# Kernel optimization log

Hardware: AMD Instinct MI355X
Metric: run time of the kernel (lower is better)

The kernel has to match this reference:

```python
import jax, jax.numpy as jnp
import numpy as np
import math

B_CH = 128   # bottleneck channels (conv1x1 in)
N_CH = 256   # encoder filters (conv1x1 out / linear in)
L = 16       # filter length (linear out); hop = L//2
BATCH = 8
K = 32000    # number of frames
T_ORIGIN = (L // 2) * (K - 1) + L  # 256008


def setup_inputs() -> dict:
    key = jax.random.key(0)
    k1, k2, k3, k4 = jax.random.split(key, 4)
    return {
        "mixture_w": jax.random.normal(k1, (BATCH, N_CH, K), jnp.float32),
        "est_mask": jax.random.normal(k2, (BATCH, B_CH, K), jnp.float32),
        "W_mask": jax.random.normal(k3, (N_CH, B_CH), jnp.float32) * (1.0 / np.sqrt(B_CH)),
        "W_basis": jax.random.normal(k4, (L, N_CH), jnp.float32) * (1.0 / np.sqrt(N_CH)),
        "T_origin": T_ORIGIN,
    }


def overlap_and_add(signal, frame_step):
    # signal: [..., frames, frame_length]
    frames, frame_length = signal.shape[-2], signal.shape[-1]
    sub_len = math.gcd(frame_length, frame_step)
    sub_step = frame_step // sub_len
    spf = frame_length // sub_len  # subframes per frame
    out_size = frame_step * (frames - 1) + frame_length
    out_sub = out_size // sub_len
    sub_sig = signal.reshape(signal.shape[:-2] + (frames * spf, sub_len))
    # scatter index for each subframe (same as torch unfold + index_add_)
    idx = (jnp.arange(frames)[:, None] * sub_step + jnp.arange(spf)[None, :]).reshape(-1)
    res = jnp.zeros(signal.shape[:-2] + (out_sub, sub_len), signal.dtype)
    res = res.at[..., idx, :].add(sub_sig)
    return res.reshape(signal.shape[:-2] + (out_size,))


def reference(mixture_w, est_mask, W_mask, W_basis, T_origin):
    # conv1x1 (bias-free) == channel matmul: [B_CH -> N_CH]
    m = jnp.einsum('nb,gbk->gnk', W_mask, est_mask)   # [batch, N, K]
    x = mixture_w * jax.nn.relu(m)                    # masked encoder output
    # transpose + Linear(N -> L, no bias): [batch, K, L]
    x = jnp.einsum('gnk,ln->gkl', x, W_basis)
    est_source = overlap_and_add(x, L // 2)           # [batch, T_conv]
    pad = T_origin - est_source.shape[-1]
    return jnp.pad(est_source, ((0, 0), (0, pad)))
```

## Files before the change

### kernel.cpp

```cpp
#include <hip/hip_runtime.h>
#include <stdint.h>

#define BATCH 8
#define NCH 256
#define BCH 128
#define KFR 32000
#define TOUT 256008
#define KT 32
#define NTILES (KFR / KT)

typedef __attribute__((ext_vector_type(8))) short bf16x8;
typedef __attribute__((ext_vector_type(4))) float f32x4;

__device__ __forceinline__ unsigned short f32_to_bf16(float f) {
    unsigned int u = __builtin_bit_cast(unsigned int, f);
    u += 0x7FFFu + ((u >> 16) & 1u);
    return (unsigned short)(u >> 16);
}
__device__ __forceinline__ float bf16_to_f32(unsigned short h) {
    unsigned int u = ((unsigned int)h) << 16;
    return __builtin_bit_cast(float, u);
}

__global__ void convert_weights(const float* __restrict__ Wm,
                                const float* __restrict__ Wb,
                                unsigned short* __restrict__ wbf) {
    int i = blockIdx.x * 256 + threadIdx.x;
    if (i < NCH * BCH) wbf[i] = f32_to_bf16(Wm[i]);
    if (i < 16 * NCH)  wbf[NCH * BCH + i] = f32_to_bf16(Wb[i]);
}

#define ESTT_STRIDE 136
#define XT_STRIDE 264
#define ESTT_BYTES (KT * ESTT_STRIDE * 2)
#define XT_BYTES (KT * XT_STRIDE * 2)
#define SMEM_BYTES (ESTT_BYTES + XT_BYTES + (8 * KT + 8) * 4)

__launch_bounds__(256, 4)
__global__ void fused_decoder(const float* __restrict__ mix,
                              const float* __restrict__ est,
                              const unsigned short* __restrict__ wbf,
                              float* __restrict__ out) {
    __shared__ __align__(16) char smem[SMEM_BYTES];
    unsigned short* estT = reinterpret_cast<unsigned short*>(smem);
    unsigned short* xt   = reinterpret_cast<unsigned short*>(smem + ESTT_BYTES);
    float* locout        = reinterpret_cast<float*>(smem + ESTT_BYTES + XT_BYTES);

    const int tid = threadIdx.x;
    const int lane = tid & 63;
    const int wv = tid >> 6;
    const int l15 = lane & 15;
    const int lq = lane >> 4;

    const int bid = blockIdx.x;
    const int g = bid / NTILES;
    const int k0 = (bid % NTILES) * KT;

    {
        const float* eg = est + ((size_t)g * BCH) * KFR + k0;
        unsigned int* dst = reinterpret_cast<unsigned int*>(estT);
#pragma unroll
        for (int it = 0; it < 2; ++it) {
            int u = it * 256 + tid;
            int f4 = u & 7;
            int bp = u >> 3;
            float4 v0 = *reinterpret_cast<const float4*>(eg + (size_t)(2 * bp) * KFR + 4 * f4);
            float4 v1 = *reinterpret_cast<const float4*>(eg + (size_t)(2 * bp + 1) * KFR + 4 * f4);
#pragma unroll
            for (int i = 0; i < 4; ++i) {
                unsigned int p = (unsigned int)f32_to_bf16((&v0.x)[i]) |
                                 ((unsigned int)f32_to_bf16((&v1.x)[i]) << 16);
                dst[(4 * f4 + i) * (ESTT_STRIDE / 2) + bp] = p;
            }
        }
    }
    __syncthreads();

    f32x4 acc[4][2];
#pragma unroll
    for (int nt = 0; nt < 4; ++nt)
#pragma unroll
        for (int ft = 0; ft < 2; ++ft) {
            f32x4 z = {0.f, 0.f, 0.f, 0.f};
            acc[nt][ft] = z;
        }
#pragma unroll
    for (int nt = 0; nt < 4; ++nt) {
        int n = 64 * wv + 16 * nt + l15;
        bf16x8 wf[4];
#pragma unroll
        for (int ks = 0; ks < 4; ++ks)
            wf[ks] = *reinterpret_cast<const bf16x8*>(wbf + n * BCH + 32 * ks + 8 * lq);
#pragma unroll
        for (int ft = 0; ft < 2; ++ft) {
            int f = 16 * ft + l15;
#pragma unroll
            for (int ks = 0; ks < 4; ++ks) {
                bf16x8 bf_ = *reinterpret_cast<const bf16x8*>(estT + f * ESTT_STRIDE + 32 * ks + 8 * lq);
                acc[nt][ft] = __builtin_amdgcn_mfma_f32_16x16x32_bf16(wf[ks], bf_, acc[nt][ft], 0, 0, 0);
            }
        }
    }
#pragma unroll
    for (int nt = 0; nt < 4; ++nt) {
        int n0 = 64 * wv + 16 * nt + 4 * lq;
#pragma unroll
        for (int ft = 0; ft < 2; ++ft) {
            int f = 16 * ft + l15;
            uint2 u;
            u.x = (unsigned int)f32_to_bf16(acc[nt][ft][0]) |
                  ((unsigned int)f32_to_bf16(acc[nt][ft][1]) << 16);
            u.y = (unsigned int)f32_to_bf16(acc[nt][ft][2]) |
                  ((unsigned int)f32_to_bf16(acc[nt][ft][3]) << 16);
            *reinterpret_cast<uint2*>(xt + f * XT_STRIDE + n0) = u;
        }
    }
    __syncthreads();

    {
        const float* mg = mix + ((size_t)g * NCH) * KFR + k0;
        unsigned int* xtd = reinterpret_cast<unsigned int*>(xt);
#pragma unroll
        for (int it = 0; it < 4; ++it) {
            int u = it * 256 + tid;
            int f4 = u & 7;
            int np = u >> 3;
            float4 v0 = *reinterpret_cast<const float4*>(mg + (size_t)(2 * np) * KFR + 4 * f4);
            float4 v1 = *reinterpret_cast<const float4*>(mg + (size_t)(2 * np + 1) * KFR + 4 * f4);
#pragma unroll
            for (int i = 0; i < 4; ++i) {
                int idx = (4 * f4 + i) * (XT_STRIDE / 2) + np;
                unsigned int p = xtd[idx];
                float m0 = bf16_to_f32((unsigned short)(p & 0xFFFFu));
                float m1 = bf16_to_f32((unsigned short)(p >> 16));
                float x0 = (m0 > 0.f) ? (&v0.x)[i] * m0 : 0.f;
                float x1 = (m1 > 0.f) ? (&v1.x)[i] * m1 : 0.f;
                xtd[idx] = (unsigned int)f32_to_bf16(x0) |
                           ((unsigned int)f32_to_bf16(x1) << 16);
            }
        }
    }
    __syncthreads();

    f32x4 acc2 = {0.f, 0.f, 0.f, 0.f};
    if (wv < 2) {
        int f = 16 * wv + l15;
#pragma unroll
        for (int ks = 0; ks < 8; ++ks) {
            bf16x8 a = *reinterpret_cast<const bf16x8*>(wbf + NCH * BCH + l15 * NCH + 32 * ks + 8 * lq);
            bf16x8 b = *reinterpret_cast<const bf16x8*>(xt + f * XT_STRIDE + 32 * ks + 8 * lq);
            acc2 = __builtin_amdgcn_mfma_f32_16x16x32_bf16(a, b, acc2, 0, 0, 0);
        }
    }

    {
        int f = 16 * wv + l15;
        int lb = 4 * lq;
        if (wv < 2 && lq < 2) {
#pragma unroll
            for (int r = 0; r < 4; ++r) locout[8 * f + lb + r] = acc2[r];
        }
        if (tid < 8) locout[256 + tid] = 0.f;
        __syncthreads();
        if (wv < 2 && lq >= 2) {
#pragma unroll
            for (int r = 0; r < 4; ++r) locout[8 * f + lb + r] += acc2[r];
        }
        __syncthreads();
    }

    {
        float* og = out + (size_t)g * TOUT + 8 * (size_t)k0;
        if (tid >= 2 && tid < 64) {
            *reinterpret_cast<float4*>(og + 4 * tid) =
                *reinterpret_cast<const float4*>(locout + 4 * tid);
        } else if (tid < 2) {
#pragma unroll
            for (int r = 0; r < 4; ++r)
                atomicAdd(og + 4 * tid + r, locout[4 * tid + r]);
        } else if (tid >= 64 && tid < 66) {
            int t = 256 + 4 * (tid - 64);
#pragma unroll
            for (int r = 0; r < 4; ++r)
                atomicAdd(og + t + r, locout[t + r]);
        }
    }
}

extern "C" void kernel_launch(void* const* d_in, const int* in_sizes, int n_in,
                              void* d_out, int out_size, void* d_ws, size_t ws_size,
                              hipStream_t stream) {
    const float* mix = (const float*)d_in[0];
    const float* est = (const float*)d_in[1];
    const float* Wm  = (const float*)d_in[2];
    const float* Wb  = (const float*)d_in[3];
    unsigned short* wbf = (unsigned short*)d_ws;

    hipMemsetAsync(d_out, 0, (size_t)out_size * sizeof(float), stream);
    convert_weights<<<128, 256, 0, stream>>>(Wm, Wb, wbf);
    fused_decoder<<<BATCH * NTILES, 256, 0, stream>>>(mix, est, wbf, (float*)d_out);
}
```

Measured before the change: 148.7 us.

## Process multiple frame tiles per block with register prefetch and swizzled LDS

Each block now loops over 8 consecutive 32-frame tiles instead of handling one. It prefetches the next tile's est_mask values into registers and issues the mixture loads before the first GEMM so global latency overlaps compute. The transposed LDS buffers use an XOR swizzle in place of padding to avoid bank conflicts. The overlap-add result stays in shared memory across tiles, which cuts atomics at tile boundaries, but the grid shrinks to 1000 blocks and register pressure rises.

New measurement: 273.3 us. +83.7%, slower.

```diff
diff --git a/kernel.cpp b/kernel.cpp
--- a/kernel.cpp
+++ b/kernel.cpp
@@ -7,7 +7,9 @@
 #define KFR 32000
 #define TOUT 256008
 #define KT 32
-#define NTILES (KFR / KT)
+#define NTPB 8
+#define CHUNK (KT * NTPB)
+#define NCHUNK (KFR / CHUNK)
 
 typedef __attribute__((ext_vector_type(8))) short bf16x8;
 typedef __attribute__((ext_vector_type(4))) float f32x4;
@@ -20,6 +22,9 @@
 __device__ __forceinline__ float bf16_to_f32(unsigned short h) {
     unsigned int u = ((unsigned int)h) << 16;
     return __builtin_bit_cast(float, u);
+}
+__device__ __forceinline__ unsigned int pack2(float a, float b) {
+    return (unsigned int)f32_to_bf16(a) | ((unsigned int)f32_to_bf16(b) << 16);
 }
 
 __global__ void convert_weights(const float* __restrict__ Wm,
@@ -30,159 +35,185 @@
     if (i < 16 * NCH)  wbf[NCH * BCH + i] = f32_to_bf16(Wb[i]);
 }
 
-#define ESTT_STRIDE 136
-#define XT_STRIDE 264
-#define ESTT_BYTES (KT * ESTT_STRIDE * 2)
-#define XT_BYTES (KT * XT_STRIDE * 2)
-#define SMEM_BYTES (ESTT_BYTES + XT_BYTES + (8 * KT + 8) * 4)
+#define ESTT_W 68
+#define XT_W 132
+#define ESTT_WORDS (KT * ESTT_W)
+#define XT_WORDS (KT * XT_W)
+#define LOC_FLOATS (8 * CHUNK + 8)
 
 __launch_bounds__(256, 4)
 __global__ void fused_decoder(const float* __restrict__ mix,
                               const float* __restrict__ est,
                               const unsigned short* __restrict__ wbf,
                               float* __restrict__ out) {
-    __shared__ __align__(16) char smem[SMEM_BYTES];
-    unsigned short* estT = reinterpret_cast<unsigned short*>(smem);
-    unsigned short* xt   = reinterpret_cast<unsigned short*>(smem + ESTT_BYTES);
-    float* locout        = reinterpret_cast<float*>(smem + ESTT_BYTES + XT_BYTES);
+    __shared__ __align__(16) unsigned int smem[ESTT_WORDS + XT_WORDS + LOC_FLOATS];
+    unsigned int* estd = smem;
+    unsigned int* xtd  = smem + ESTT_WORDS;
+    unsigned short* estT = reinterpret_cast<unsigned short*>(estd);
+    unsigned short* xt   = reinterpret_cast<unsigned short*>(xtd);
+    float* locout = reinterpret_cast<float*>(smem + ESTT_WORDS + XT_WORDS);
 
     const int tid = threadIdx.x;
     const int lane = tid & 63;
     const int wv = tid >> 6;
     const int l15 = lane & 15;
     const int lq = lane >> 4;
+    const int f4 = tid & 7;
+    const int rbase = tid >> 3;
 
     const int bid = blockIdx.x;
-    const int g = bid / NTILES;
-    const int k0 = (bid % NTILES) * KT;
+    const int g = bid / NCHUNK;
+    const int c = bid % NCHUNK;
+
+    const float* eg0 = est + ((size_t)g * BCH) * KFR + c * CHUNK;
+    const float* mg0 = mix + ((size_t)g * NCH) * KFR + c * CHUNK;
+
+    for (int s = tid; s < LOC_FLOATS / 4; s += 256) {
+        float4 z = {0.f, 0.f, 0.f, 0.f};
+        *reinterpret_cast<float4*>(locout + 4 * s) = z;
+    }
+
+    float4 er[2][2];
+#pragma unroll
+    for (int it = 0; it < 2; ++it) {
+        int bp = it * 32 + rbase;
+        er[it][0] = *reinterpret_cast<const float4*>(eg0 + (size_t)(2 * bp) * KFR + 4 * f4);
+        er[it][1] = *reinterpret_cast<const float4*>(eg0 + (size_t)(2 * bp + 1) * KFR + 4 * f4);
+    }
+
+    for (int t = 0; t < NTPB; ++t) {
+        const float* mg = mg0 + t * KT;
+        const float* egn = eg0 + (t + 1 < NTPB ? (t + 1) * KT : t * KT);
+
+        {
+            int msk = (f4 >> 1) & 3;
+#pragma unroll
+            for (int it = 0; it < 2; ++it) {
+                int bp = it * 32 + rbase;
+                int base = (((bp >> 2) ^ msk) << 2) + (bp & 3);
+#pragma unroll
+                for (int i = 0; i < 4; ++i) {
+                    unsigned int p = pack2((&er[it][0].x)[i], (&er[it][1].x)[i]);
+                    estd[(4 * f4 + i) * ESTT_W + base] = p;
+                }
+            }
+        }
+#pragma unroll
+        for (int it = 0; it < 2; ++it) {
+            int bp = it * 32 + rbase;
+            er[it][0] = *reinterpret_cast<const float4*>(egn + (size_t)(2 * bp) * KFR + 4 * f4);
+            er[it][1] = *reinterpret_cast<const float4*>(egn + (size_t)(2 * bp + 1) * KFR + 4 * f4);
+        }
+        float4 mr[4][2];
+#pragma unroll
+        for (int it = 0; it < 4; ++it) {
+            int np = it * 32 + rbase;
+            mr[it][0] = *reinterpret_cast<const float4*>(mg + (size_t)(2 * np) * KFR + 4 * f4);
+            mr[it][1] = *reinterpret_cast<const float4*>(mg + (size_t)(2 * np + 1) * KFR + 4 * f4);
+        }
+        __syncthreads();
+
+        f32x4 acc[4][2];
+#pragma unroll
+        for (int nt = 0; nt < 4; ++nt)
+#pragma unroll
+            for (int ft = 0; ft < 2; ++ft) {
+                f32x4 z = {0.f, 0.f, 0.f, 0.f};
+                acc[nt][ft] = z;
+            }
+#pragma unroll
+        for (int nt = 0; nt < 4; ++nt) {
+            int n = 64 * wv + 16 * nt + l15;
+            bf16x8 wf[4];
+#pragma unroll
+            for (int ks = 0; ks < 4; ++ks)
+                wf[ks] = *reinterpret_cast<const bf16x8*>(wbf + n * BCH + 32 * ks + 8 * lq);
+#pragma unroll
+            for (int ft = 0; ft < 2; ++ft) {
+                int f = 16 * ft + l15;
+                int msk = (2 * ft + (l15 >> 3)) & 3;
+#pragma unroll
+                for (int ks = 0; ks < 4; ++ks) {
+                    bf16x8 b = *reinterpret_cast<const bf16x8*>(
+                        estT + f * (2 * ESTT_W) + 8 * ((4 * ks + lq) ^ msk));
+                    acc[nt][ft] = __builtin_amdgcn_mfma_f32_16x16x32_bf16(wf[ks], b, acc[nt][ft], 0, 0, 0);
+                }
+            }
+        }
+#pragma unroll
+        for (int nt = 0; nt < 4; ++nt)
+#pragma unroll
+            for (int ft = 0; ft < 2; ++ft) {
+                int f = 16 * ft + l15;
+                int msk = (2 * ft + (l15 >> 3)) & 3;
+                int v = 8 * wv + 2 * nt + (lq >> 1);
+                int word = f * XT_W + (((v ^ msk) << 2)) + 2 * (lq & 1);
+                uint2 u;
+                u.x = pack2(acc[nt][ft][0], acc[nt][ft][1]);
+                u.y = pack2(acc[nt][ft][2], acc[nt][ft][3]);
+                *reinterpret_cast<uint2*>(xtd + word) = u;
+            }
+        __syncthreads();
+
+        {
+            int msk = (f4 >> 1) & 3;
+#pragma unroll
+            for (int it = 0; it < 4; ++it) {
+                int np = it * 32 + rbase;
+                int base = (((np >> 2) ^ msk) << 2) + (np & 3);
+#pragma unroll
+                for (int i = 0; i < 4; ++i) {
+                    int idx = (4 * f4 + i) * XT_W + base;
+                    unsigned int p = xtd[idx];
+                    float m0 = bf16_to_f32((unsigned short)(p & 0xFFFFu));
+                    float m1 = bf16_to_f32((unsigned short)(p >> 16));
+                    float x0 = (m0 > 0.f) ? (&mr[it][0].x)[i] * m0 : 0.f;
+                    float x1 = (m1 > 0.f) ? (&mr[it][1].x)[i] * m1 : 0.f;
+                    xtd[idx] = pack2(x0, x1);
+                }
+            }
+        }
+        __syncthreads();
+
+        f32x4 acc2 = {0.f, 0.f, 0.f, 0.f};
+        if (wv < 2) {
+            int f = 16 * wv + l15;
+            int msk = (2 * wv + (l15 >> 3)) & 3;
+#pragma unroll
+            for (int ks = 0; ks < 8; ++ks) {
+                bf16x8 a = *reinterpret_cast<const bf16x8*>(
+                    wbf + NCH * BCH + l15 * NCH + 32 * ks + 8 * lq);
+                bf16x8 b = *reinterpret_cast<const bf16x8*>(
+                    xt + f * (2 * XT_W) + 8 * ((4 * ks + lq) ^ msk));
+                acc2 = __builtin_amdgcn_mfma_f32_16x16x32_bf16(a, b, acc2, 0, 0, 0);
+            }
+        }
+        if (wv < 2 && lq < 2) {
+            int f = 16 * wv + l15;
+            int base = 256 * t + 8 * f + 4 * lq;
+#pragma unroll
+            for (int r = 0; r < 4; ++r) locout[base + r] += acc2[r];
+        }
+        __syncthreads();
+        if (wv < 2 && lq >= 2) {
+            int f = 16 * wv + l15;
+            int base = 256 * t + 8 * f + 4 * lq;
+#pragma unroll
+            for (int r = 0; r < 4; ++r) locout[base + r] += acc2[r];
+        }
+    }
+    __syncthreads();
 
     {
-        const float* eg = est + ((size_t)g * BCH) * KFR + k0;
-        unsigned int* dst = reinterpret_cast<unsigned int*>(estT);
-#pragma unroll
-        for (int it = 0; it < 2; ++it) {
-            int u = it * 256 + tid;
-            int f4 = u & 7;
-            int bp = u >> 3;
-            float4 v0 = *reinterpret_cast<const float4*>(eg + (size_t)(2 * bp) * KFR + 4 * f4);
-            float4 v1 = *reinterpret_cast<const float4*>(eg + (size_t)(2 * bp + 1) * KFR + 4 * f4);
-#pragma unroll
-            for (int i = 0; i < 4; ++i) {
-                unsigned int p = (unsigned int)f32_to_bf16((&v0.x)[i]) |
-                                 ((unsigned int)f32_to_bf16((&v1.x)[i]) << 16);
-                dst[(4 * f4 + i) * (ESTT_STRIDE / 2) + bp] = p;
-            }
-        }
-    }
-    __syncthreads();
-
-    f32x4 acc[4][2];
-#pragma unroll
-    for (int nt = 0; nt < 4; ++nt)
-#pragma unroll
-        for (int ft = 0; ft < 2; ++ft) {
-            f32x4 z = {0.f, 0.f, 0.f, 0.f};
-            acc[nt][ft] = z;
-        }
-#pragma unroll
-    for (int nt = 0; nt < 4; ++nt) {
-        int n = 64 * wv + 16 * nt + l15;
-        bf16x8 wf[4];
-#pragma unroll
-        for (int ks = 0; ks < 4; ++ks)
-            wf[ks] = *reinterpret_cast<const bf16x8*>(wbf + n * BCH + 32 * ks + 8 * lq);
-#pragma unroll
-        for (int ft = 0; ft < 2; ++ft) {
-            int f = 16 * ft + l15;
-#pragma unroll
-            for (int ks = 0; ks < 4; ++ks) {
-                bf16x8 bf_ = *reinterpret_cast<const bf16x8*>(estT + f * ESTT_STRIDE + 32 * ks + 8 * lq);
-                acc[nt][ft] = __builtin_amdgcn_mfma_f32_16x16x32_bf16(wf[ks], bf_, acc[nt][ft], 0, 0, 0);
-            }
-        }
-    }
-#pragma unroll
-    for (int nt = 0; nt < 4; ++nt) {
-        int n0 = 64 * wv + 16 * nt + 4 * lq;
-#pragma unroll
-        for (int ft = 0; ft < 2; ++ft) {
-            int f = 16 * ft + l15;
-            uint2 u;
-            u.x = (unsigned int)f32_to_bf16(acc[nt][ft][0]) |
-                  ((unsigned int)f32_to_bf16(acc[nt][ft][1]) << 16);
-            u.y = (unsigned int)f32_to_bf16(acc[nt][ft][2]) |
-                  ((unsigned int)f32_to_bf16(acc[nt][ft][3]) << 16);
-            *reinterpret_cast<uint2*>(xt + f * XT_STRIDE + n0) = u;
-        }
-    }
-    __syncthreads();
-
-    {
-        const float* mg = mix + ((size_t)g * NCH) * KFR + k0;
-        unsigned int* xtd = reinterpret_cast<unsigned int*>(xt);
-#pragma unroll
-        for (int it = 0; it < 4; ++it) {
-            int u = it * 256 + tid;
-            int f4 = u & 7;
-            int np = u >> 3;
-            float4 v0 = *reinterpret_cast<const float4*>(mg + (size_t)(2 * np) * KFR + 4 * f4);
-            float4 v1 = *reinterpret_cast<const float4*>(mg + (size_t)(2 * np + 1) * KFR + 4 * f4);
-#pragma unroll
-            for (int i = 0; i < 4; ++i) {
-                int idx = (4 * f4 + i) * (XT_STRIDE / 2) + np;
-                unsigned int p = xtd[idx];
-                float m0 = bf16_to_f32((unsigned short)(p & 0xFFFFu));
-                float m1 = bf16_to_f32((unsigned short)(p >> 16));
-                float x0 = (m0 > 0.f) ? (&v0.x)[i] * m0 : 0.f;
-                float x1 = (m1 > 0.f) ? (&v1.x)[i] * m1 : 0.f;
-                xtd[idx] = (unsigned int)f32_to_bf16(x0) |
-                           ((unsigned int)f32_to_bf16(x1) << 16);
-            }
-        }
-    }
-    __syncthreads();
-
-    f32x4 acc2 = {0.f, 0.f, 0.f, 0.f};
-    if (wv < 2) {
-        int f = 16 * wv + l15;
-#pragma unroll
-        for (int ks = 0; ks < 8; ++ks) {
-            bf16x8 a = *reinterpret_cast<const bf16x8*>(wbf + NCH * BCH + l15 * NCH + 32 * ks + 8 * lq);
-            bf16x8 b = *reinterpret_cast<const bf16x8*>(xt + f * XT_STRIDE + 32 * ks + 8 * lq);
-            acc2 = __builtin_amdgcn_mfma_f32_16x16x32_bf16(a, b, acc2, 0, 0, 0);
-        }
-    }
-
-    {
-        int f = 16 * wv + l15;
-        int lb = 4 * lq;
-        if (wv < 2 && lq < 2) {
-#pragma unroll
-            for (int r = 0; r < 4; ++r) locout[8 * f + lb + r] = acc2[r];
-        }
-        if (tid < 8) locout[256 + tid] = 0.f;
-        __syncthreads();
-        if (wv < 2 && lq >= 2) {
-#pragma unroll
-            for (int r = 0; r < 4; ++r) locout[8 * f + lb + r] += acc2[r];
-        }
-        __syncthreads();
-    }
-
-    {
-        float* og = out + (size_t)g * TOUT + 8 * (size_t)k0;
-        if (tid >= 2 && tid < 64) {
-            *reinterpret_cast<float4*>(og + 4 * tid) =
-                *reinterpret_cast<const float4*>(locout + 4 * tid);
-        } else if (tid < 2) {
-#pragma unroll
-            for (int r = 0; r < 4; ++r)
-                atomicAdd(og + 4 * tid + r, locout[4 * tid + r]);
-        } else if (tid >= 64 && tid < 66) {
-            int t = 256 + 4 * (tid - 64);
-#pragma unroll
-            for (int r = 0; r < 4; ++r)
-                atomicAdd(og + t + r, locout[t + r]);
+        float* og = out + (size_t)g * TOUT + (size_t)(8 * CHUNK) * c;
+        for (int s = tid; s < LOC_FLOATS / 4; s += 256) {
+            float4 v = *reinterpret_cast<const float4*>(locout + 4 * s);
+            if (s >= 2 && s < (LOC_FLOATS / 4 - 2)) {
+                *reinterpret_cast<float4*>(og + 4 * s) = v;
+            } else {
+#pragma unroll
+                for (int r = 0; r < 4; ++r) atomicAdd(og + 4 * s + r, (&v.x)[r]);
+            }
         }
     }
 }
@@ -198,5 +229,5 @@
 
     hipMemsetAsync(d_out, 0, (size_t)out_size * sizeof(float), stream);
     convert_weights<<<128, 256, 0, stream>>>(Wm, Wb, wbf);
-    fused_decoder<<<BATCH * NTILES, 256, 0, stream>>>(mix, est, wbf, (float*)d_out);
-}
+    fused_decoder<<<BATCH * NCHUNK, 256, 0, stream>>>(mix, est, wbf, (float*)d_out);
+}
```
